# Kernel tuning notes

Hardware: AMD Instinct MI355X
Metric: run time of the kernel (lower is better)

## Reference

```python
import jax, jax.numpy as jnp
import numpy as np

# ---- static dims (from init_kwargs) ----
B, V, G, NH, C = 2, 3, 2, 8, 128
CPG, CH, HPG = C // G, C // NH, NH // G          # 64, 16, 4
Hq = Wq = 32
D = 4                                            # bev_depth_dim
Hk, Wk = Hq // 2, Wq * D                         # 16, 128 (per rearrange)
NS = Hk * Wk                                     # n_sample = 2048
Hi = Wi = 64
SCALE = CH ** -0.5
OFR = 5.0                                        # offset_range_factor
EPS = 1e-5


def grid_sample_bilinear(img, grid):
    """torch.F.grid_sample(mode='bilinear', align_corners=True, padding='zeros').
    img: (N, Cc, H, W); grid: (N, Hg, Wg, 2) with (x, y) in [-1, 1]."""
    N, Cc, H, W = img.shape
    x = (grid[..., 0] + 1.0) * 0.5 * (W - 1)
    y = (grid[..., 1] + 1.0) * 0.5 * (H - 1)
    x0 = jnp.floor(x); y0 = jnp.floor(y)
    wx1 = x - x0; wy1 = y - y0
    wx0 = 1.0 - wx1; wy0 = 1.0 - wy1

    def gather(ix, iy):
        valid = ((ix >= 0) & (ix <= W - 1) & (iy >= 0) & (iy <= H - 1)).astype(img.dtype)
        ixc = jnp.clip(ix, 0, W - 1).astype(jnp.int32)
        iyc = jnp.clip(iy, 0, H - 1).astype(jnp.int32)
        vals = jax.vmap(lambda im, yy, xx: im[:, yy, xx])(img, iyc, ixc)  # (N,Cc,Hg,Wg)
        return vals * valid[:, None]

    return (gather(x0, y0) * (wx0 * wy0)[:, None]
            + gather(x0 + 1.0, y0) * (wx1 * wy0)[:, None]
            + gather(x0, y0 + 1.0) * (wx0 * wy1)[:, None]
            + gather(x0 + 1.0, y0 + 1.0) * (wx1 * wy1)[:, None])


def offset_net(qg, w1, b1, gln, bln, w2):
    """Depthwise 1x1 conv (groups=CPG, fan-out D) -> channel LayerNorm -> GELU -> 1x1 conv.
    qg: (B*G, CPG, Hq, Wq) -> (B*G, D, Hq, Wq)."""
    h = qg[:, :, None] * w1.reshape(CPG, D)[None, :, :, None, None] \
        + b1.reshape(CPG, D)[None, :, :, None, None]
    h = h.reshape(B * G, CPG * D, Hq, Wq)
    mu = h.mean(axis=1, keepdims=True)
    var = h.var(axis=1, keepdims=True)           # biased, like torch LayerNorm
    h = (h - mu) * jax.lax.rsqrt(var + EPS) * gln[None, :, None, None] + bln[None, :, None, None]
    h = jax.nn.gelu(h, approximate=False)
    return jnp.einsum('oc,bchw->bohw', w2, h)


def _q_grid():
    gy, gx = jnp.meshgrid(jnp.linspace(-1.0, 1.0, Hq), jnp.linspace(-1.0, 1.0, Wq), indexing='ij')
    return jnp.stack([gy, gx], -1)               # (Hq, Wq, 2) in (y, x)


def setup_inputs() -> dict:
    key = jax.random.key(0)
    ks = jax.random.split(key, 15)
    s = 0.05
    return {
        'x': jax.random.normal(ks[0], (B, V, C, Hi, Wi), jnp.float32),
        'query': jax.random.normal(ks[1], (B, C, Hq, Wq), jnp.float32),
        'reference_points': jax.random.uniform(ks[2], (B, V, Hk, Wk, 2), jnp.float32) * 2.0 - 1.0,
        'off_w1': jax.random.normal(ks[3], (V, CPG * D), jnp.float32) * s,
        'off_b1': jax.random.normal(ks[4], (V, CPG * D), jnp.float32) * s,
        'off_ln_g': jnp.ones((V, CPG * D), jnp.float32),
        'off_ln_b': jnp.zeros((V, CPG * D), jnp.float32),
        'off_w2': jax.random.normal(ks[5], (V, D, CPG * D), jnp.float32) * s,
        'k_w': jax.random.normal(ks[6], (C, C), jnp.float32) * s,
        'k_b': jnp.zeros((C,), jnp.float32),
        'v_w': jax.random.normal(ks[7], (C, C), jnp.float32) * s,
        'v_b': jnp.zeros((C,), jnp.float32),
        'out_w': jax.random.normal(ks[8], (C, C * V), jnp.float32) * s,
        'out_b': jnp.zeros((C,), jnp.float32),
        'rpe_table': jax.random.normal(ks[9], (NH, Hq * 2 - 1, Wq * D * 2 - 1), jnp.float32) * 0.01,
    }


def reference(x, query, reference_points, off_w1, off_b1, off_ln_g, off_ln_b, off_w2,
              k_w, k_b, v_w, v_b, out_w, out_b, rpe_table):
    ref = reference_points[..., ::-1]                     # (x,y) -> (y,x)
    ref = jnp.repeat(ref, G, axis=0)                      # (B*G, V, Hk, Wk, 2)
    q_g = query.reshape(B, G, CPG, Hq, Wq).reshape(B * G, CPG, Hq, Wq)
    q = query.reshape(B * NH, CH, Hq * Wq)
    qg = _q_grid().reshape(1, Hq * Wq, 2)
    off_rng = jnp.array([1.0 / (Hk - 1.0), 1.0 / (Wk - 1.0)], jnp.float32).reshape(1, 2, 1, 1)
    rpe = jnp.broadcast_to(rpe_table[None], (B,) + rpe_table.shape)
    rpe = rpe.reshape(B * G, HPG, rpe_table.shape[1], rpe_table.shape[2])

    outs = []
    for vi in range(V):
        off = offset_net(q_g, off_w1[vi], off_b1[vi], off_ln_g[vi], off_ln_b[vi], off_w2[vi])
        # rearrange '(b g) d (h n) w -> (b g) n h (w d)'
        off = off.reshape(B * G, D, Hk, 2, Wq).transpose(0, 3, 2, 4, 1).reshape(B * G, 2, Hk, Wk)
        off = jnp.tanh(off) * off_rng * OFR
        off = off.transpose(0, 2, 3, 1)                   # (B*G, Hk, Wk, 2) in (y, x)
        rwo = off + ref[:, vi]                            # scale_offset_range=True -> no clamp
        xs = grid_sample_bilinear(x[:, vi].reshape(B * G, CPG, Hi, Wi), rwo[..., ::-1])
        xs = xs.reshape(B, C, NS)
        k = (jnp.einsum('oc,bcn->bon', k_w, xs) + k_b[None, :, None]).reshape(B * NH, CH, NS)
        vv = (jnp.einsum('oc,bcn->bon', v_w, xs) + v_b[None, :, None]).reshape(B * NH, CH, NS)
        attn = jnp.einsum('bcm,bcn->bmn', q, k) * SCALE   # (B*NH, m, NS)
        disp = (qg[:, :, None] - rwo.reshape(B * G, NS, 2)[:, None]) * 0.5  # (B*G, m, NS, 2)
        bias = grid_sample_bilinear(rpe, disp[..., ::-1]).reshape(B * NH, Hq * Wq, NS)
        attn = jax.nn.softmax(attn + bias, axis=-1)
        outs.append(jnp.einsum('bmn,bcn->bcm', attn, vv).reshape(B, C, Hq, Wq))

    out = jnp.concatenate(outs, axis=1)                   # (B, V*C, Hq, Wq)
    return jnp.einsum('oc,bchw->bohw', out_w, out) + out_b[None, :, None, None]
```

## Files before the change

kernel.cpp:

```cpp
#include <hip/hip_runtime.h>
#include <hip/hip_bf16.h>
#include <math.h>


typedef __attribute__((ext_vector_type(8))) short short8;
typedef __attribute__((ext_vector_type(4))) float f32x4;

__device__ __forceinline__ unsigned short f2b(float f){
  unsigned u = __float_as_uint(f);
  return (unsigned short)((u + 0x7FFFu + ((u>>16)&1u)) >> 16);
}
__device__ __forceinline__ unsigned cvt_pk_bf16(float lo, float hi){
  unsigned r;
  asm("v_cvt_pk_bf16_f32 %0, %1, %2" : "=v"(r) : "v"(lo), "v"(hi));
  return r;
}

__global__ void k_probe(float* __restrict__ out, float code){
  if(blockIdx.x==0 && threadIdx.x==0) out[0] = code;
}

__global__ __launch_bounds__(256) void k_prep_off(
    const float* __restrict__ query, const float* __restrict__ refp,
    const float* __restrict__ w1, const float* __restrict__ b1,
    const float* __restrict__ lng, const float* __restrict__ lnb,
    const float* __restrict__ w2, float* __restrict__ rwo, float* __restrict__ rws,
    const float* __restrict__ x, float* __restrict__ xt,
    const float* __restrict__ k_w, const float* __restrict__ v_w, const float* __restrict__ out_w,
    unsigned short* __restrict__ kw16, unsigned short* __restrict__ vw16, float* __restrict__ ow_t){
  __shared__ float t[64][65];
  int bx = blockIdx.x;
  if(bx < 3072){
    int wid  = bx*4 + (threadIdx.x>>6);
    int lane = threadIdx.x & 63;
    int vi  = wid >> 12;
    int rem = wid & 4095;
    int bg  = rem >> 10;
    int pix = rem & 1023;
    int y = pix >> 5, xq = pix & 31;
    int b = bg >> 1, g = bg & 1;
    float qv = query[(size_t)(b*128 + g*64 + lane)*1024 + pix];
    float h[4]; float s1 = 0.f, s2 = 0.f;
    #pragma unroll
    for(int d=0; d<4; ++d){
      h[d] = qv*w1[vi*256 + lane*4 + d] + b1[vi*256 + lane*4 + d];
      s1 += h[d]; s2 += h[d]*h[d];
    }
    #pragma unroll
    for(int off=1; off<64; off<<=1){ s1 += __shfl_xor(s1, off); s2 += __shfl_xor(s2, off); }
    float mu   = s1 * (1.f/256.f);
    float var  = s2 * (1.f/256.f) - mu*mu;
    float rstd = rsqrtf(fmaxf(var, 0.f) + 1e-5f);
    float po[4] = {0.f,0.f,0.f,0.f};
    #pragma unroll
    for(int d=0; d<4; ++d){
      float hv = (h[d]-mu)*rstd*lng[vi*256+lane*4+d] + lnb[vi*256+lane*4+d];
      hv = 0.5f*hv*(1.f + erff(hv*0.70710678118654752f));
      #pragma unroll
      for(int o=0; o<4; ++o) po[o] += w2[(vi*4+o)*256 + lane*4 + d] * hv;
    }
    #pragma unroll
    for(int off=1; off<64; off<<=1){
      #pragma unroll
      for(int o=0; o<4; ++o) po[o] += __shfl_xor(po[o], off);
    }
    if(lane == 0){
      int tt = y & 1, hk = y >> 1;
      float rng = tt ? (5.f/127.f) : (5.f/15.f);
      float csc = tt ? 63.5f : 15.5f;
      #pragma unroll
      for(int d=0; d<4; ++d){
        int wk = xq*4 + d;
        float rv = refp[(size_t)(((b*3+vi)*16 + hk)*128 + wk)*2 + (1-tt)];
        float coord = tanhf(po[d])*rng + rv;
        size_t o2 = ((size_t)(vi*4+bg)*2048 + hk*128 + wk)*2 + tt;
        rwo[o2] = coord;
        rws[o2] = coord * csc;
      }
    }
  } else if(bx < 3840){
    int pb = bx - 3072;
    int iy = pb & 63;
    int o2 = pb >> 6;
    const float* src = x + ((size_t)o2*64)*4096 + (size_t)iy*64;
    int ix = threadIdx.x & 63, cq = threadIdx.x >> 6;
    #pragma unroll
    for(int c0 = 0; c0 < 64; c0 += 4)
      t[c0+cq][ix] = src[(size_t)(c0+cq)*4096 + ix];
    __syncthreads();
    float* dst = xt + (((size_t)o2*64 + iy)*64)*64;
    int c = threadIdx.x & 63, xq = threadIdx.x >> 6;
    #pragma unroll
    for(int x0 = 0; x0 < 64; x0 += 4)
      dst[(size_t)(x0+xq)*64 + c] = t[c][x0+xq];
  } else {
    int wb = bx - 3840;
    if(wb < 128){
      int i = (wb & 63)*256 + threadIdx.x;
      if(wb < 64) kw16[i] = f2b(k_w[i]);
      else        vw16[i] = f2b(v_w[i]);
    } else {
      int i = (wb-128)*256 + threadIdx.x;
      if(i < 49152){
        int r = i / 384, c = i - r*384;
        ow_t[c*128 + r] = out_w[i];
      }
    }
  }
}

__global__ __launch_bounds__(256) void k_sampro(
    const float* __restrict__ rwo, const float* __restrict__ xt,
    const unsigned short* __restrict__ kw16, const float* __restrict__ k_b,
    const unsigned short* __restrict__ vw16, const float* __restrict__ v_b,
    unsigned short* __restrict__ k_b16, unsigned short* __restrict__ v_t16){
  __shared__ alignas(16) unsigned short tile[16*136];
  int bx = blockIdx.x;
  int nt = bx & 127;
  int r2 = bx >> 7;
  int b = r2 & 1, vi = r2 >> 1;
  int n0 = nt*16;
  int tid = threadIdx.x, wid = tid>>6, lane = tid&63;
  #pragma unroll
  for(int s = 0; s < 8; ++s){
    int u = wid*8 + s;
    int nl = u >> 1, g = u & 1;
    int n = n0 + nl;
    float yn = rwo[((size_t)(vi*4 + b*2 + g)*2048 + n)*2 + 0];
    float xn = rwo[((size_t)(vi*4 + b*2 + g)*2048 + n)*2 + 1];
    float px = (xn + 1.f)*31.5f;
    float py = (yn + 1.f)*31.5f;
    float x0 = floorf(px), y0 = floorf(py);
    float fx = px - x0, fy = py - y0;
    int ix0 = (int)x0, iy0 = (int)y0;
    const float* base = xt + (size_t)((b*3+vi)*2+g)*4096*64;
    float wts[4] = {(1.f-fx)*(1.f-fy), fx*(1.f-fy), (1.f-fx)*fy, fx*fy};
    int ixs[4] = {ix0, ix0+1, ix0, ix0+1};
    int iys[4] = {iy0, iy0, iy0+1, iy0+1};
    float acc = 0.f;
    #pragma unroll
    for(int tp=0; tp<4; ++tp){
      int ix = ixs[tp], iy = iys[tp];
      if(ix>=0 && ix<64 && iy>=0 && iy<64)
        acc += wts[tp] * base[(size_t)((iy<<6)+ix)*64 + lane];
    }
    tile[nl*136 + g*64 + lane] = f2b(acc);
  }
  __syncthreads();
  int c = lane & 15, qd = lane >> 4;
  short8 af[4];
  #pragma unroll
  for(int kc=0; kc<4; ++kc)
    af[kc] = *(const short8*)(&tile[c*136 + kc*32 + qd*8]);
  size_t vbbase = (size_t)(vi*16 + b*8)*2048*16;
  const float SC2 = 0.36067376022224085f;
  #pragma unroll
  for(int half=0; half<2; ++half){
    int nh = wid*2 + half;
    size_t hbase = vbbase + (size_t)nh*2048*16;
    {
      f32x4 C = {0.f,0.f,0.f,0.f};
      #pragma unroll
      for(int kc=0; kc<4; ++kc){
        short8 bf = *(const short8*)(kw16 + (size_t)(nh*16 + c)*128 + kc*32 + qd*8);
        C = __builtin_amdgcn_mfma_f32_16x16x32_bf16(af[kc], bf, C, 0, 0, 0);
      }
      float bias = k_b[nh*16 + c];
      #pragma unroll
      for(int r=0; r<4; ++r)
        k_b16[hbase + (size_t)(n0 + qd*4 + r)*16 + c] = f2b((C[r] + bias)*SC2);
    }
    {
      f32x4 C = {0.f,0.f,0.f,0.f};
      #pragma unroll
      for(int kc=0; kc<4; ++kc){
        short8 bf = *(const short8*)(vw16 + (size_t)(nh*16 + c)*128 + kc*32 + qd*8);
        C = __builtin_amdgcn_mfma_f32_16x16x32_bf16(af[kc], bf, C, 0, 0, 0);
      }
      float bias = v_b[nh*16 + c];
      uint2 pk;
      pk.x = cvt_pk_bf16(C[0]+bias, C[1]+bias);
      pk.y = cvt_pk_bf16(C[2]+bias, C[3]+bias);
      *(uint2*)(v_t16 + hbase + (size_t)c*2048 + n0 + qd*4) = pk;
    }
  }
}

__global__ __launch_bounds__(512,6) void k_attn(
    const float* __restrict__ rws, const unsigned short* __restrict__ k_b16,
    const unsigned short* __restrict__ v_t16, const float* __restrict__ query,
    const float* __restrict__ rpe, float* __restrict__ attn_pc){
  __shared__ unsigned P32[49*197];
  __shared__ alignas(16) short p_sm[8][16*40];
  int bx = blockIdx.x;
  int vi = bx >> 8;
  int bh = (bx >> 4) & 15;
  int mq = (bx >> 1) & 7;
  int h  = bx & 1;
  int b = bh >> 3, nh = bh & 7, g = nh >> 2, bg = b*2 + g;
  int tid = threadIdx.x, wid = tid >> 6;
  int w4  = wid & 3;
  int nhf = wid >> 2;
  int lane = tid & 63, c = lane & 15, qd = lane >> 4;
  int m0 = (mq*4 + w4)*32 + 16*h;
  int xoff = h*64;
  float gy0 = -1.f + (2.f/31.f)*(float)(mq*4);
  float pyL = 15.5f*(gy0 - 4.f/3.f) + 31.f - 0.01f;
  float pyH = 15.5f*(gy0 + 6.f/31.f + 4.f/3.f) + 31.f + 0.01f;
  int a  = max(-1, (int)floorf(pyL));
  int bb = min(63, (int)floorf(pyH));
  int iy_lo = max(a - 1, bb - 48);
  {
    const float* rt = rpe + (size_t)nh*16065;
    for(int e = tid; e < 49*197; e += 512){
      int rr = e / 197;
      int cc = e - rr*197;
      int iy = iy_lo + rr;
      int ix = cc - 1 + xoff;
      bool xv = (ix >= 0) && (ix <= 254);
      float lo = (xv && iy   >= 0 && iy   <= 62) ? rt[iy*255 + ix]     : 0.f;
      float hi = (xv && iy+1 >= 0 && iy+1 <= 62) ? rt[(iy+1)*255 + ix] : 0.f;
      P32[e] = cvt_pk_bf16(lo*1.44269504f, (hi - lo)*1.44269504f);
    }
  }
  short8 qa;
  #pragma unroll
  for(int j=0; j<8; ++j){
    int ch = qd*8 + j;
    qa[j] = (qd < 2) ? (short)f2b(query[(size_t)(b*128 + nh*16 + ch)*1024 + m0 + c]) : (short)0;
  }
  float Ax2[4];
  #pragma unroll
  for(int r=0; r<4; ++r){
    int mr = m0 + qd*4 + r;
    float gxr = -1.f + (2.f/31.f)*(mr & 31);
    Ax2[r] = 63.5f*gxr + 128.f;
  }
  float gyw = -1.f + (2.f/31.f)*(float)(m0 >> 5);
  float Ay  = 15.5f*gyw + 31.f - (float)iy_lo;
  float loC = fmaxf(-1.f - (float)iy_lo, 0.f);
  float hiC = fminf(63.f - (float)iy_lo, 47.f);
  float pxLo = (float)xoff, pxHi = (float)(xoff + 192);
  float si[4] = {0.f, 0.f, 0.f, 0.f};
  f32x4 O = {0.f, 0.f, 0.f, 0.f};
  size_t kvb  = (size_t)(vi*16 + bh)*2048*16;
  size_t rwsb = (size_t)(vi*4 + bg)*2048;
  short* pw = &p_sm[wid][0];
  const f32x4 z = {0.f,0.f,0.f,0.f};
  __syncthreads();
  for(int nc = nhf*8, ncE = nhf*8 + 8; nc < ncE; ++nc){
    int n0 = nc*128;
    const unsigned short* kb = k_b16 + kvb + (size_t)(n0 + c)*16 + qd*8;
    f32x4 S0, S1, N0, N1;
    {
      short8 bk0 = {0,0,0,0,0,0,0,0}, bk1 = {0,0,0,0,0,0,0,0};
      if(qd < 2){ bk0 = *(const short8*)(kb); bk1 = *(const short8*)(kb + 256); }
      N0 = __builtin_amdgcn_mfma_f32_16x16x32_bf16(qa, bk0, z, 0, 0, 0);
      N1 = __builtin_amdgcn_mfma_f32_16x16x32_bf16(qa, bk1, z, 0, 0, 0);
    }
    #pragma unroll
    for(int kc=0; kc<4; ++kc){
      S0 = N0; S1 = N1;
      if(kc < 3){
        short8 bk0 = {0,0,0,0,0,0,0,0}, bk1 = {0,0,0,0,0,0,0,0};
        if(qd < 2){ bk0 = *(const short8*)(kb + (2*kc+2)*256); bk1 = *(const short8*)(kb + (2*kc+3)*256); }
        N0 = __builtin_amdgcn_mfma_f32_16x16x32_bf16(qa, bk0, z, 0, 0, 0);
        N1 = __builtin_amdgcn_mfma_f32_16x16x32_bf16(qa, bk1, z, 0, 0, 0);
      }
      float pe[4], po[4];
      {
        float2 rs = *(const float2*)(rws + (rwsb + n0 + (2*kc)*16 + c)*2);
        float py = Ay - rs.x;
        py = fminf(fmaxf(py, loC), hiC);
        float rf = floorf(py);
        float fy = py - rf;
        int rbase = (int)rf * 197;
        #pragma unroll
        for(int r=0; r<4; ++r){
          float px = Ax2[r] - rs.y;
          px = fminf(fmaxf(px, pxLo), pxHi);
          float cf = floorf(px);
          float fx = px - cf;
          int idx = rbase + (int)cf + 1 - xoff;
          unsigned w0 = P32[idx], w1 = P32[idx+1];
          float lo0 = __uint_as_float(w0 << 16), d0 = __uint_as_float(w0 & 0xFFFF0000u);
          float lo1 = __uint_as_float(w1 << 16), d1 = __uint_as_float(w1 & 0xFFFF0000u);
          float t0 = lo0 + fy*d0;
          float t1 = lo1 + fy*d1;
          float p = exp2f(S0[r] + t0 + fx*(t1 - t0));
          si[r] += p;
          pe[r] = p;
        }
      }
      {
        float2 rs = *(const float2*)(rws + (rwsb + n0 + (2*kc+1)*16 + c)*2);
        float py = Ay - rs.x;
        py = fminf(fmaxf(py, loC), hiC);
        float rf = floorf(py);
        float fy = py - rf;
        int rbase = (int)rf * 197;
        #pragma unroll
        for(int r=0; r<4; ++r){
          float px = Ax2[r] - rs.y;
          px = fminf(fmaxf(px, pxLo), pxHi);
          float cf = floorf(px);
          float fx = px - cf;
          int idx = rbase + (int)cf + 1 - xoff;
          unsigned w0 = P32[idx], w1 = P32[idx+1];
          float lo0 = __uint_as_float(w0 << 16), d0 = __uint_as_float(w0 & 0xFFFF0000u);
          float lo1 = __uint_as_float(w1 << 16), d1 = __uint_as_float(w1 & 0xFFFF0000u);
          float t0 = lo0 + fy*d0;
          float t1 = lo1 + fy*d1;
          float p = exp2f(S1[r] + t0 + fx*(t1 - t0));
          si[r] += p;
          po[r] = p;
        }
      }
      #pragma unroll
      for(int r=0; r<4; ++r){
        unsigned pk = cvt_pk_bf16(pe[r], po[r]);
        pw[(qd*4 + r)*40 + c]      = (short)pk;
        pw[(qd*4 + r)*40 + 16 + c] = (short)(pk >> 16);
      }
      short8 va = *(const short8*)(v_t16 + kvb + (size_t)c*2048 + n0 + kc*32 + qd*8);
      short8 pbf = *(const short8*)(&pw[c*40 + qd*8]);
      O = __builtin_amdgcn_mfma_f32_16x16x32_bf16(va, pbf, O, 0, 0, 0);
    }
  }
  __syncthreads();
  float* red = (float*)&p_sm[0][0];
  int basei = (w4*64 + lane)*8;
  if(nhf){
    red[basei+0] = O[0];  red[basei+1] = O[1];
    red[basei+2] = O[2];  red[basei+3] = O[3];
    red[basei+4] = si[0]; red[basei+5] = si[1];
    red[basei+6] = si[2]; red[basei+7] = si[3];
  }
  __syncthreads();
  if(!nhf){
    O[0] += red[basei+0]; O[1] += red[basei+1];
    O[2] += red[basei+2]; O[3] += red[basei+3];
    si[0] += red[basei+4]; si[1] += red[basei+5];
    si[2] += red[basei+6]; si[3] += red[basei+7];
    #pragma unroll
    for(int r=0; r<4; ++r){
      float sv = si[r];
      sv += __shfl_xor(sv, 1); sv += __shfl_xor(sv, 2);
      sv += __shfl_xor(sv, 4); sv += __shfl_xor(sv, 8);
      si[r] = sv;
    }
    int msrc = (c >> 2)*16 + c;
    int rsel = c & 3;
    float s0 = __shfl(si[0], msrc), s1 = __shfl(si[1], msrc),
          s2 = __shfl(si[2], msrc), s3 = __shfl(si[3], msrc);
    float sv = (rsel==0) ? s0 : ((rsel==1) ? s1 : ((rsel==2) ? s2 : s3));
    float inv = 1.f/sv;
    float4 o4;
    o4.x = O[0]*inv; o4.y = O[1]*inv; o4.z = O[2]*inv; o4.w = O[3]*inv;
    *(float4*)(attn_pc + (size_t)(b*1024 + m0 + c)*384 + vi*128 + nh*16 + qd*4) = o4;
  }
}

__global__ __launch_bounds__(256) void k_outproj(
    const float* __restrict__ attn_pc, const float* __restrict__ ow_t, const float* __restrict__ out_b,
    float* __restrict__ out){
  __shared__ float A[4*384];
  int bx = blockIdx.x;
  int b  = bx >> 8;
  int m0 = (bx & 255)*4;
  const float4* src = (const float4*)(attn_pc + ((size_t)b*1024 + m0)*384);
  float4* dst = (float4*)A;
  for(int i = threadIdx.x; i < 384; i += 256) dst[i] = src[i];
  __syncthreads();
  int oc = threadIdx.x & 127;
  int mh = threadIdx.x >> 7;
  float acc[2] = {0.f,0.f};
  #pragma unroll 4
  for(int vc = 0; vc < 384; ++vc){
    float wv = ow_t[vc*128 + oc];
    #pragma unroll
    for(int j=0; j<2; ++j) acc[j] += wv * A[(mh*2+j)*384 + vc];
  }
  float ob = out_b[oc];
  #pragma unroll
  for(int j=0; j<2; ++j)
    out[((size_t)b*128 + oc)*1024 + m0 + mh*2 + j] = acc[j] + ob;
}

extern "C" void kernel_launch(void* const* d_in, const int* in_sizes, int n_in,
                              void* d_out, int out_size, void* d_ws, size_t ws_size,
                              hipStream_t stream){
  const float* x     = (const float*)d_in[0];
  const float* query = (const float*)d_in[1];
  const float* refp  = (const float*)d_in[2];
  const float* w1    = (const float*)d_in[3];
  const float* b1    = (const float*)d_in[4];
  const float* lng   = (const float*)d_in[5];
  const float* lnb   = (const float*)d_in[6];
  const float* w2    = (const float*)d_in[7];
  const float* k_w   = (const float*)d_in[8];
  const float* k_b   = (const float*)d_in[9];
  const float* v_w   = (const float*)d_in[10];
  const float* v_b   = (const float*)d_in[11];
  const float* out_w = (const float*)d_in[12];
  const float* out_b = (const float*)d_in[13];
  const float* rpe   = (const float*)d_in[14];

  const size_t O_XT   = 0;
  const size_t O_RWO  = 12582912;
  const size_t O_RWS  = 12779520;
  const size_t O_KB16 = 12976128;
  const size_t O_VT16 = 16121856;
  const size_t O_APC  = 19267584;
  const size_t O_KW16 = 22413312;
  const size_t O_VW16 = 22446080;
  const size_t O_OWT  = 22478848;
  const size_t NEED   = 22675456;
  if(ws_size < NEED){
    k_probe<<<1, 64, 0, stream>>>((float*)d_out, 100.f + (float)(ws_size >> 20));
    return;
  }
  char* ws = (char*)d_ws;
  float* xt      = (float*)(ws + O_XT);
  float* rwo     = (float*)(ws + O_RWO);
  float* rws     = (float*)(ws + O_RWS);
  unsigned short* k_b16 = (unsigned short*)(ws + O_KB16);
  unsigned short* v_t16 = (unsigned short*)(ws + O_VT16);
  float* attn_pc = (float*)(ws + O_APC);
  unsigned short* kw16 = (unsigned short*)(ws + O_KW16);
  unsigned short* vw16 = (unsigned short*)(ws + O_VW16);
  float* ow_t    = (float*)(ws + O_OWT);

  k_prep_off<<<4160, 256, 0, stream>>>(query, refp, w1, b1, lng, lnb, w2, rwo, rws,
                                       x, xt, k_w, v_w, out_w, kw16, vw16, ow_t);
  k_sampro  <<<768,  256, 0, stream>>>(rwo, xt, kw16, k_b, vw16, v_b, k_b16, v_t16);
  k_attn    <<<768,  512, 0, stream>>>(rws, k_b16, v_t16, query, rpe, attn_pc);
  k_outproj <<<512,  256, 0, stream>>>(attn_pc, ow_t, out_b, (float*)d_out);
}
```

Before: 248.9 us.

## Widen sampling kernel to 512 threads and simplify attention bias indexing

The sampling/projection kernel now runs with 512 threads per block, so each wave does half the bilinear samples and a single head's K/V projection instead of two. This adds parallelism per block. In the attention kernel, the x-offset is folded into the per-row constants, which simplifies clamping and LDS index arithmetic. The software-pipelined QK MFMA prefetch is removed in favour of straight per-chunk MFMAs, with exp2 batched after the bias interpolation. That trades explicit MFMA/ALU overlap for lower register pressure and simpler code.

```diff
diff --git a/kernel.cpp b/kernel.cpp
--- a/kernel.cpp
+++ b/kernel.cpp
@@ -109,7 +109,7 @@
   }
 }
 
-__global__ __launch_bounds__(256) void k_sampro(
+__global__ __launch_bounds__(512) void k_sampro(
     const float* __restrict__ rwo, const float* __restrict__ xt,
     const unsigned short* __restrict__ kw16, const float* __restrict__ k_b,
     const unsigned short* __restrict__ vw16, const float* __restrict__ v_b,
@@ -122,8 +122,8 @@
   int n0 = nt*16;
   int tid = threadIdx.x, wid = tid>>6, lane = tid&63;
   #pragma unroll
-  for(int s = 0; s < 8; ++s){
-    int u = wid*8 + s;
+  for(int s = 0; s < 4; ++s){
+    int u = wid*4 + s;
     int nl = u >> 1, g = u & 1;
     int n = n0 + nl;
     float yn = rwo[((size_t)(vi*4 + b*2 + g)*2048 + n)*2 + 0];
@@ -154,35 +154,32 @@
     af[kc] = *(const short8*)(&tile[c*136 + kc*32 + qd*8]);
   size_t vbbase = (size_t)(vi*16 + b*8)*2048*16;
   const float SC2 = 0.36067376022224085f;
-  #pragma unroll
-  for(int half=0; half<2; ++half){
-    int nh = wid*2 + half;
-    size_t hbase = vbbase + (size_t)nh*2048*16;
-    {
-      f32x4 C = {0.f,0.f,0.f,0.f};
-      #pragma unroll
-      for(int kc=0; kc<4; ++kc){
-        short8 bf = *(const short8*)(kw16 + (size_t)(nh*16 + c)*128 + kc*32 + qd*8);
-        C = __builtin_amdgcn_mfma_f32_16x16x32_bf16(af[kc], bf, C, 0, 0, 0);
-      }
-      float bias = k_b[nh*16 + c];
-      #pragma unroll
-      for(int r=0; r<4; ++r)
-        k_b16[hbase + (size_t)(n0 + qd*4 + r)*16 + c] = f2b((C[r] + bias)*SC2);
-    }
-    {
-      f32x4 C = {0.f,0.f,0.f,0.f};
-      #pragma unroll
-      for(int kc=0; kc<4; ++kc){
-        short8 bf = *(const short8*)(vw16 + (size_t)(nh*16 + c)*128 + kc*32 + qd*8);
-        C = __builtin_amdgcn_mfma_f32_16x16x32_bf16(af[kc], bf, C, 0, 0, 0);
-      }
-      float bias = v_b[nh*16 + c];
-      uint2 pk;
-      pk.x = cvt_pk_bf16(C[0]+bias, C[1]+bias);
-      pk.y = cvt_pk_bf16(C[2]+bias, C[3]+bias);
-      *(uint2*)(v_t16 + hbase + (size_t)c*2048 + n0 + qd*4) = pk;
-    }
+  int nh = wid;
+  size_t hbase = vbbase + (size_t)nh*2048*16;
+  {
+    f32x4 C = {0.f,0.f,0.f,0.f};
+    #pragma unroll
+    for(int kc=0; kc<4; ++kc){
+      short8 bf = *(const short8*)(kw16 + (size_t)(nh*16 + c)*128 + kc*32 + qd*8);
+      C = __builtin_amdgcn_mfma_f32_16x16x32_bf16(af[kc], bf, C, 0, 0, 0);
+    }
+    float bias = k_b[nh*16 + c];
+    #pragma unroll
+    for(int r=0; r<4; ++r)
+      k_b16[hbase + (size_t)(n0 + qd*4 + r)*16 + c] = f2b((C[r] + bias)*SC2);
+  }
+  {
+    f32x4 C = {0.f,0.f,0.f,0.f};
+    #pragma unroll
+    for(int kc=0; kc<4; ++kc){
+      short8 bf = *(const short8*)(vw16 + (size_t)(nh*16 + c)*128 + kc*32 + qd*8);
+      C = __builtin_amdgcn_mfma_f32_16x16x32_bf16(af[kc], bf, C, 0, 0, 0);
+    }
+    float bias = v_b[nh*16 + c];
+    uint2 pk;
+    pk.x = cvt_pk_bf16(C[0]+bias, C[1]+bias);
+    pk.y = cvt_pk_bf16(C[2]+bias, C[3]+bias);
+    *(uint2*)(v_t16 + hbase + (size_t)c*2048 + n0 + qd*4) = pk;
   }
 }
 
@@ -234,13 +231,12 @@
   for(int r=0; r<4; ++r){
     int mr = m0 + qd*4 + r;
     float gxr = -1.f + (2.f/31.f)*(mr & 31);
-    Ax2[r] = 63.5f*gxr + 128.f;
+    Ax2[r] = 63.5f*gxr + 128.f - (float)xoff;
   }
   float gyw = -1.f + (2.f/31.f)*(float)(m0 >> 5);
   float Ay  = 15.5f*gyw + 31.f - (float)iy_lo;
   float loC = fmaxf(-1.f - (float)iy_lo, 0.f);
   float hiC = fminf(63.f - (float)iy_lo, 47.f);
-  float pxLo = (float)xoff, pxHi = (float)(xoff + 192);
   float si[4] = {0.f, 0.f, 0.f, 0.f};
   f32x4 O = {0.f, 0.f, 0.f, 0.f};
   size_t kvb  = (size_t)(vi*16 + bh)*2048*16;
@@ -251,45 +247,33 @@
   for(int nc = nhf*8, ncE = nhf*8 + 8; nc < ncE; ++nc){
     int n0 = nc*128;
     const unsigned short* kb = k_b16 + kvb + (size_t)(n0 + c)*16 + qd*8;
-    f32x4 S0, S1, N0, N1;
-    {
+    #pragma unroll
+    for(int kc=0; kc<4; ++kc){
       short8 bk0 = {0,0,0,0,0,0,0,0}, bk1 = {0,0,0,0,0,0,0,0};
-      if(qd < 2){ bk0 = *(const short8*)(kb); bk1 = *(const short8*)(kb + 256); }
-      N0 = __builtin_amdgcn_mfma_f32_16x16x32_bf16(qa, bk0, z, 0, 0, 0);
-      N1 = __builtin_amdgcn_mfma_f32_16x16x32_bf16(qa, bk1, z, 0, 0, 0);
-    }
-    #pragma unroll
-    for(int kc=0; kc<4; ++kc){
-      S0 = N0; S1 = N1;
-      if(kc < 3){
-        short8 bk0 = {0,0,0,0,0,0,0,0}, bk1 = {0,0,0,0,0,0,0,0};
-        if(qd < 2){ bk0 = *(const short8*)(kb + (2*kc+2)*256); bk1 = *(const short8*)(kb + (2*kc+3)*256); }
-        N0 = __builtin_amdgcn_mfma_f32_16x16x32_bf16(qa, bk0, z, 0, 0, 0);
-        N1 = __builtin_amdgcn_mfma_f32_16x16x32_bf16(qa, bk1, z, 0, 0, 0);
-      }
-      float pe[4], po[4];
+      if(qd < 2){ bk0 = *(const short8*)(kb + (2*kc)*256); bk1 = *(const short8*)(kb + (2*kc+1)*256); }
+      f32x4 S0 = __builtin_amdgcn_mfma_f32_16x16x32_bf16(qa, bk0, z, 0, 0, 0);
+      f32x4 S1 = __builtin_amdgcn_mfma_f32_16x16x32_bf16(qa, bk1, z, 0, 0, 0);
+      float be[4], bo[4];
       {
         float2 rs = *(const float2*)(rws + (rwsb + n0 + (2*kc)*16 + c)*2);
         float py = Ay - rs.x;
         py = fminf(fmaxf(py, loC), hiC);
         float rf = floorf(py);
         float fy = py - rf;
-        int rbase = (int)rf * 197;
+        int rbase = (int)rf * 197 + 1;
         #pragma unroll
         for(int r=0; r<4; ++r){
           float px = Ax2[r] - rs.y;
-          px = fminf(fmaxf(px, pxLo), pxHi);
+          px = fminf(fmaxf(px, 0.f), 192.f);
           float cf = floorf(px);
           float fx = px - cf;
-          int idx = rbase + (int)cf + 1 - xoff;
+          int idx = rbase + (int)cf;
           unsigned w0 = P32[idx], w1 = P32[idx+1];
           float lo0 = __uint_as_float(w0 << 16), d0 = __uint_as_float(w0 & 0xFFFF0000u);
           float lo1 = __uint_as_float(w1 << 16), d1 = __uint_as_float(w1 & 0xFFFF0000u);
           float t0 = lo0 + fy*d0;
           float t1 = lo1 + fy*d1;
-          float p = exp2f(S0[r] + t0 + fx*(t1 - t0));
-          si[r] += p;
-          pe[r] = p;
+          be[r] = t0 + fx*(t1 - t0);
         }
       }
       {
@@ -298,24 +282,27 @@
         py = fminf(fmaxf(py, loC), hiC);
         float rf = floorf(py);
         float fy = py - rf;
-        int rbase = (int)rf * 197;
+        int rbase = (int)rf * 197 + 1;
         #pragma unroll
         for(int r=0; r<4; ++r){
           float px = Ax2[r] - rs.y;
-          px = fminf(fmaxf(px, pxLo), pxHi);
+          px = fminf(fmaxf(px, 0.f), 192.f);
           float cf = floorf(px);
           float fx = px - cf;
-          int idx = rbase + (int)cf + 1 - xoff;
+          int idx = rbase + (int)cf;
           unsigned w0 = P32[idx], w1 = P32[idx+1];
           float lo0 = __uint_as_float(w0 << 16), d0 = __uint_as_float(w0 & 0xFFFF0000u);
           float lo1 = __uint_as_float(w1 << 16), d1 = __uint_as_float(w1 & 0xFFFF0000u);
           float t0 = lo0 + fy*d0;
           float t1 = lo1 + fy*d1;
-          float p = exp2f(S1[r] + t0 + fx*(t1 - t0));
-          si[r] += p;
-          po[r] = p;
+          bo[r] = t0 + fx*(t1 - t0);
         }
       }
+      float pe[4], po[4];
+      #pragma unroll
+      for(int r=0; r<4; ++r){ pe[r] = exp2f(S0[r] + be[r]); si[r] += pe[r]; }
+      #pragma unroll
+      for(int r=0; r<4; ++r){ po[r] = exp2f(S1[r] + bo[r]); si[r] += po[r]; }
       #pragma unroll
       for(int r=0; r<4; ++r){
         unsigned pk = cvt_pk_bf16(pe[r], po[r]);
@@ -433,7 +420,7 @@
 
   k_prep_off<<<4160, 256, 0, stream>>>(query, refp, w1, b1, lng, lnb, w2, rwo, rws,
                                        x, xt, k_w, v_w, out_w, kw16, vw16, ow_t);
-  k_sampro  <<<768,  256, 0, stream>>>(rwo, xt, kw16, k_b, vw16, v_b, k_b16, v_t16);
+  k_sampro  <<<768,  512, 0, stream>>>(rwo, xt, kw16, k_b, vw16, v_b, k_b16, v_t16);
   k_attn    <<<768,  512, 0, stream>>>(rws, k_b16, v_t16, query, rpe, attn_pc);
   k_outproj <<<512,  256, 0, stream>>>(attn_pc, ow_t, out_b, (float*)d_out);
 }
```

Result: faster. 240.3 us (-3.5%).
